# Performance work log

Hardware: AMD Instinct MI355X
Metric: run time of the kernel (lower is better)

Reference implementation:

```python
import jax, jax.numpy as jnp
import numpy as np

# --- fixed model configuration (from init_kwargs) ---
Nx, Nu, Ny, Np = 3, 1, 2, 5
Nz = Np * (Ny + Nu)          # 15
F, V, DELTA = 0.1, 1.0, 1.0  # ps (flow), volume, sampling time
CAMEAN, CBMEAN = 0.5, 0.4    # yscale means
CASTD, CBSTD = 0.3, 0.2      # yscale stds
CAFMEAN, CAFSTD = 1.0, 0.5   # uscale


def _fnn(x, W1, b1, W2, b2):
    # dense(tanh) -> dense(linear), as createDenseLayers/fnnTf
    return jnp.tanh(x @ W1 + b1) @ W2 + b2


def setup_inputs() -> dict:
    B, T = 4096, 1024
    key = jax.random.key(0)
    ks = jax.random.split(key, 16)
    g = lambda k, shp, fan: (jax.random.normal(k, shp, jnp.float32) / np.sqrt(fan))
    return {
        "u": jax.random.normal(ks[0], (B, T, Nu), jnp.float32),
        "xz0": jax.random.normal(ks[1], (B, Nx + Nz), jnp.float32),
        "r1_W1": g(ks[2], (1, 16), 1),  "r1_b1": jnp.zeros((16,), jnp.float32),
        "r1_W2": g(ks[3], (16, 1), 16), "r1_b2": jnp.zeros((1,), jnp.float32),
        "r2_W1": g(ks[4], (2, 16), 2),  "r2_b1": jnp.zeros((16,), jnp.float32),
        "r2_W2": g(ks[5], (16, 1), 16), "r2_b2": jnp.zeros((1,), jnp.float32),
        "eC_W1": g(ks[6], (Nz, 32), Nz), "eC_b1": jnp.zeros((32,), jnp.float32),
        "eC_W2": g(ks[7], (32, 1), 32),  "eC_b2": jnp.zeros((1,), jnp.float32),
    }


def _forward(u, xz0, r1_W1, r1_b1, r1_W2, r1_b2,
             r2_W1, r2_b1, r2_W2, r2_b2, eC_W1, eC_b1, eC_W2, eC_b2):

    def fxu(x, uu):
        Ca, Cb, Cc = x[:, 0:1], x[:, 1:2], x[:, 2:3]
        Caf = uu[:, 0:1]
        r1 = _fnn(Ca, r1_W1, r1_b1, r1_W2, r1_b2) * CASTD
        r2 = _fnn(jnp.concatenate((Cb, Cc), -1), r2_W1, r2_b1, r2_W2, r2_b2) * CBSTD
        Ca = Ca * CASTD + CAMEAN
        Cb = Cb * CBSTD + CBMEAN
        Cc = Cc * CBSTD + CBMEAN
        Caf = Caf * CAFSTD + CAFMEAN
        dCa = F * (Caf - Ca) / V - r1
        dCb = -F * Cb / V + r1 - 3.0 * r2
        dCc = -F * Cc / V + r2
        return jnp.concatenate([dCa / CASTD, dCb / CBSTD, dCc / CBSTD], -1)

    # initial state: replace Cc with NN estimate from past data z0
    y0 = xz0[:, :Ny]
    z0 = xz0[:, Nx:]
    Cc0 = _fnn(z0, eC_W1, eC_b1, eC_W2, eC_b2)
    xz = jnp.concatenate((y0, Cc0, z0), -1)  # [B, Nx+Nz]

    def step(xz, uu):
        x, z = xz[:, :Nx], xz[:, Nx:]
        ypseq, upseq = z[:, :Np * Ny], z[:, Np * Ny:]
        k1 = fxu(x, uu)
        k2 = fxu(x + DELTA * (k1 / 2.0), uu)
        k3 = fxu(x + DELTA * (k2 / 2.0), uu)
        k4 = fxu(x + DELTA * k3, uu)
        xplus = x + (DELTA / 6.0) * (k1 + 2.0 * k2 + 2.0 * k3 + k4)
        zplus = jnp.concatenate((ypseq[:, Ny:], x[:, :Ny], upseq[:, Nu:], uu), -1)
        CcNN = _fnn(z, eC_W1, eC_b1, eC_W2, eC_b2)
        y = jnp.concatenate((x, CcNN), -1)  # [B, Nx+1]
        return jnp.concatenate((xplus, zplus), -1), y

    u_t = jnp.swapaxes(u, 0, 1)  # [T, B, Nu]
    _, ys = jax.lax.scan(step, xz, u_t)
    yseq_full = jnp.swapaxes(ys, 0, 1)      # [B, T, Nx+1]
    yseq = yseq_full[..., :Ny]
    xseq = yseq_full[..., :Nx]
    return yseq_full, yseq, xseq


def reference(u, xz0, r1_W1, r1_b1, r1_W2, r1_b2,
              r2_W1, r2_b1, r2_W2, r2_b2, eC_W1, eC_b1, eC_W2, eC_b2):
    return _forward(u, xz0, r1_W1, r1_b1, r1_W2, r1_b2,
                    r2_W1, r2_b1, r2_W2, r2_b2, eC_W1, eC_b1, eC_W2, eC_b2)
```

## Files before the change

kernel.cpp:

```cpp
#include <hip/hip_runtime.h>
#include <stdint.h>
#include <math.h>

#define NB 4096
#define NT 1024


#if __has_builtin(__builtin_amdgcn_exp2f)
#define EXP2F __builtin_amdgcn_exp2f
#else
#define EXP2F exp2f
#endif
#if __has_builtin(__builtin_amdgcn_rcpf)
#define RCPF __builtin_amdgcn_rcpf
#else
#define RCPF(x) (1.0f / (x))
#endif

#define TS 2.885390081777927f

typedef float f32x2 __attribute__((ext_vector_type(2)));
__device__ __forceinline__ f32x2 sp2(float s) { return (f32x2){s, s}; }
#define FMA2(a, b, c) __builtin_elementwise_fma((a), (b), (c))

template <int CTRL>
__device__ __forceinline__ float dppmov(float x) {
  return __int_as_float(
      __builtin_amdgcn_update_dpp(0, __float_as_int(x), CTRL, 0xF, 0xF, true));
}

__global__ __launch_bounds__(64) void phase1_kernel(
    const float* __restrict__ u, const float* __restrict__ xz0,
    const float* __restrict__ r1W1, const float* __restrict__ r1b1,
    const float* __restrict__ r1W2, const float* __restrict__ r1b2,
    const float* __restrict__ r2W1, const float* __restrict__ r2b1,
    const float* __restrict__ r2W2, const float* __restrict__ r2b2,
    const float* __restrict__ eCW1, const float* __restrict__ eCb1,
    const float* __restrict__ eCW2, const float* __restrict__ eCb2,
    float* __restrict__ out) {
  const int tid = threadIdx.x;
  const int cl = tid & 7;
  const int q = tid & 3;
  const bool isQ1 = (tid & 4) != 0;
  const int chain = (blockIdx.x << 3) + (tid >> 3);

  f32x2 wAv0, wAv1, wBv0, wBv1, wCv0, wCv1, wPn2v0, wPn2v1;
  float wPsum;
  {
    float wa[4], wb[4], wc[4], wp[4];
#pragma unroll
    for (int m = 0; m < 4; ++m) {
      const int un = q + 4 * m;
      if (!isQ1) {
        wa[m] = r1W1[un] * TS;
        wb[m] = 0.0f;
        wc[m] = r1b1[un] * TS;
        wp[m] = r1W2[un];
      } else {
        wa[m] = r2W1[un] * TS;
        wb[m] = r2W1[16 + un] * TS;
        wc[m] = r2b1[un] * TS;
        wp[m] = r2W2[un];
      }
    }
    wAv0 = (f32x2){wa[0], wa[1]};
    wAv1 = (f32x2){wa[2], wa[3]};
    wBv0 = (f32x2){wb[0], wb[1]};
    wBv1 = (f32x2){wb[2], wb[3]};
    wCv0 = (f32x2){wc[0], wc[1]};
    wCv1 = (f32x2){wc[2], wc[3]};
    wPn2v0 = (f32x2){-2.0f * wp[0], -2.0f * wp[1]};
    wPn2v1 = (f32x2){-2.0f * wp[2], -2.0f * wp[3]};
    wPsum = wp[0] + wp[1] + wp[2] + wp[3];
  }
  const f32x2 wPh = {wPsum, 0.0f};
  const f32x2 zero2 = {0.0f, 0.0f};

  const f32x2 cwAh0 = 0.5f * wAv0, cwAh1 = 0.5f * wAv1;
  const f32x2 cwAf0 = wAv0, cwAf1 = wAv1;
  const f32x2 cwBh0 = 0.5f * wBv0, cwBh1 = 0.5f * wBv1;
  const f32x2 cwBf0 = wBv0, cwBf1 = wBv1;
  const f32x2 eOWNh0 =
      isQ1 ? (0.5f * wBv0 - 1.5f * wAv0) : (-0.5f * wAv0);
  const f32x2 eOWNh1 =
      isQ1 ? (0.5f * wBv1 - 1.5f * wAv1) : (-0.5f * wAv1);
  const f32x2 eOWNf0 = isQ1 ? (wBv0 - 3.0f * wAv0) : (-wAv0);
  const f32x2 eOWNf1 = isQ1 ? (wBv1 - 3.0f * wAv1) : (-wAv1);
  const f32x2 eOTHh0 = isQ1 ? (0.75f * wAv0) : zero2;
  const f32x2 eOTHh1 = isQ1 ? (0.75f * wAv1) : zero2;
  const f32x2 eOTHf0 = isQ1 ? (1.5f * wAv0) : zero2;
  const f32x2 eOTHf1 = isQ1 ? (1.5f * wAv1) : zero2;

  const float c1 = r1b2[0];
  const float c2 = r2b2[0];
  const float C0b = 1.0f / 6.0f - c1;
  const float C1 = -0.2f + 1.5f * c1 - 3.0f * c2;
  const float C2 = c2 - 0.2f;

  const float* xzr = xz0 + chain * 18;
  float x0 = xzr[0];
  float x1 = xzr[1];
  float x2;

  {
    float eh[4], ewn2[4];
    float ewsum = 0.0f;
#pragma unroll
    for (int m = 0; m < 4; ++m) {
      const int un = 4 * cl + m;
      eh[m] = eCb1[un];
      ewn2[m] = -2.0f * eCW2[un];
      ewsum += eCW2[un];
    }
#pragma unroll
    for (int i = 0; i < 15; ++i) {
      const float z = xzr[3 + i];
#pragma unroll
      for (int m = 0; m < 4; ++m)
        eh[m] = __builtin_fmaf(z, eCW1[i * 32 + 4 * cl + m], eh[m]);
    }
    float pl = ewsum;
#pragma unroll
    for (int m = 0; m < 4; ++m) {
      const float e = EXP2F(eh[m] * TS);
      const float r = RCPF(e + 1.0f);
      pl = __builtin_fmaf(ewn2[m], r, pl);
    }
    pl += dppmov<0xB1>(pl);
    pl += dppmov<0x4E>(pl);
    pl = pl + dppmov<0x141>(pl);
    x2 = pl + eCb2[0];
  }

  size_t idx0;
  int stride;
  if (cl < 3) {
    idx0 = (size_t)chain * NT * 4 + cl;
    stride = 4;
  } else if (cl < 5) {
    idx0 = (size_t)NB * NT * 4 + (size_t)chain * NT * 2 + (cl - 3);
    stride = 2;
  } else {
    idx0 = (size_t)NB * NT * 6 + (size_t)chain * NT * 3 + (cl - 5);
    stride = 3;
  }
  float* sp = out + idx0;
  const bool selx0 = (cl == 0) || (cl == 3) || (cl == 5);
  const bool selx1 = (cl == 1) || (cl == 4) || (cl == 6);

  auto nets = [&](f32x2 h0, f32x2 h1, float& Sown, float& Soth) {
    f32x2 e0, e1, r01, r23;
    e0.x = EXP2F(h0.x);
    e0.y = EXP2F(h0.y);
    e1.x = EXP2F(h1.x);
    e1.y = EXP2F(h1.y);
    e0 = e0 + sp2(1.0f);
    e1 = e1 + sp2(1.0f);
    r01.x = RCPF(e0.x);
    r01.y = RCPF(e0.y);
    r23.x = RCPF(e1.x);
    r23.y = RCPF(e1.y);
    f32x2 acc = FMA2(wPn2v0, r01, wPh);
    acc = FMA2(wPn2v1, r23, acc);
    float pl = acc.x + acc.y;
    pl += dppmov<0xB1>(pl);
    pl += dppmov<0x4E>(pl);
    Sown = pl;
    Soth = dppmov<0x141>(pl);
  };

  const float* urow = u + (size_t)chain * NT;
  float4 ucur = *(const float4*)urow;
  for (int t4 = 0; t4 < NT; t4 += 4) {
    const int tn = (t4 + 4 < NT) ? (t4 + 4) : (NT - 4);
    const float4 unext = *(const float4*)(urow + tn);
    const float us4[4] = {ucur.x, ucur.y, ucur.z, ucur.w};
#pragma unroll
    for (int e = 0; e < 4; ++e) {
      const float v = selx0 ? x0 : (selx1 ? x1 : x2);
      *sp = v;
      sp += stride;
      const float C0t = __builtin_fmaf(us4[e], 1.0f / 6.0f, C0b);
      const float U0 = __builtin_fmaf(-0.1f, x0, C0t);
      const float U1 = __builtin_fmaf(-0.1f, x1, C1);
      const float U2 = __builtin_fmaf(-0.1f, x2, C2);
      const float sU = isQ1 ? x1 : x0;
      const float sV = isQ1 ? x2 : x0;
      const f32x2 hx0 = FMA2(sp2(sU), wAv0, FMA2(sp2(sV), wBv0, wCv0));
      const f32x2 hx1 = FMA2(sp2(sU), wAv1, FMA2(sp2(sV), wBv1, wCv1));
      float So, St, S1, S2;
      nets(hx0, hx1, So, St);
      S1 = isQ1 ? St : So;
      S2 = isQ1 ? So : St;
      const float k10 = U0 - S1;
      const float k11 =
          __builtin_fmaf(1.5f, S1, __builtin_fmaf(-3.0f, S2, U1));
      const float k12 = U2 + S2;
      {
        const float Ua = isQ1 ? U1 : U0;
        const f32x2 p0 = FMA2(cwAh0, sp2(Ua), FMA2(cwBh0, sp2(U2), hx0));
        const f32x2 p1 = FMA2(cwAh1, sp2(Ua), FMA2(cwBh1, sp2(U2), hx1));
        const f32x2 h0 = FMA2(eOTHh0, sp2(St), FMA2(eOWNh0, sp2(So), p0));
        const f32x2 h1 = FMA2(eOTHh1, sp2(St), FMA2(eOWNh1, sp2(So), p1));
        nets(h0, h1, So, St);
      }
      const float U0_2 = __builtin_fmaf(-0.05f, k10, U0);
      const float U1_2 = __builtin_fmaf(-0.05f, k11, U1);
      const float U2_2 = __builtin_fmaf(-0.05f, k12, U2);
      S1 = isQ1 ? St : So;
      S2 = isQ1 ? So : St;
      const float k20 = U0_2 - S1;
      const float k21 =
          __builtin_fmaf(1.5f, S1, __builtin_fmaf(-3.0f, S2, U1_2));
      const float k22 = U2_2 + S2;
      {
        const float Ua = isQ1 ? U1_2 : U0_2;
        const f32x2 p0 = FMA2(cwAh0, sp2(Ua), FMA2(cwBh0, sp2(U2_2), hx0));
        const f32x2 p1 = FMA2(cwAh1, sp2(Ua), FMA2(cwBh1, sp2(U2_2), hx1));
        const f32x2 h0 = FMA2(eOTHh0, sp2(St), FMA2(eOWNh0, sp2(So), p0));
        const f32x2 h1 = FMA2(eOTHh1, sp2(St), FMA2(eOWNh1, sp2(So), p1));
        nets(h0, h1, So, St);
      }
      const float U0_3 = __builtin_fmaf(-0.05f, k20, U0);
      const float U1_3 = __builtin_fmaf(-0.05f, k21, U1);
      const float U2_3 = __builtin_fmaf(-0.05f, k22, U2);
      S1 = isQ1 ? St : So;
      S2 = isQ1 ? So : St;
      const float k30 = U0_3 - S1;
      const float k31 =
          __builtin_fmaf(1.5f, S1, __builtin_fmaf(-3.0f, S2, U1_3));
      const float k32 = U2_3 + S2;
      {
        const float Ua = isQ1 ? U1_3 : U0_3;
        const f32x2 p0 = FMA2(cwAf0, sp2(Ua), FMA2(cwBf0, sp2(U2_3), hx0));
        const f32x2 p1 = FMA2(cwAf1, sp2(Ua), FMA2(cwBf1, sp2(U2_3), hx1));
        const f32x2 h0 = FMA2(eOTHf0, sp2(St), FMA2(eOWNf0, sp2(So), p0));
        const f32x2 h1 = FMA2(eOTHf1, sp2(St), FMA2(eOWNf1, sp2(So), p1));
        nets(h0, h1, So, St);
      }
      const float U0_4 = __builtin_fmaf(-0.1f, k30, U0);
      const float U1_4 = __builtin_fmaf(-0.1f, k31, U1);
      const float U2_4 = __builtin_fmaf(-0.1f, k32, U2);
      S1 = isQ1 ? St : So;
      S2 = isQ1 ? So : St;
      const float k40 = U0_4 - S1;
      const float k41 =
          __builtin_fmaf(1.5f, S1, __builtin_fmaf(-3.0f, S2, U1_4));
      const float k42 = U2_4 + S2;
      float tA = k20 + k30;
      tA = __builtin_fmaf(2.0f, tA, k10) + k40;
      x0 = __builtin_fmaf(1.0f / 6.0f, tA, x0);
      float tB = k21 + k31;
      tB = __builtin_fmaf(2.0f, tB, k11) + k41;
      x1 = __builtin_fmaf(1.0f / 6.0f, tB, x1);
      float tC = k22 + k32;
      tC = __builtin_fmaf(2.0f, tC, k12) + k42;
      x2 = __builtin_fmaf(1.0f / 6.0f, tC, x2);
    }
    ucur = unext;
  }
}

__global__ __launch_bounds__(256) void phase2_kernel(
    const float* __restrict__ u, const float* __restrict__ xz0,
    const float* __restrict__ eCW1, const float* __restrict__ eCb1,
    const float* __restrict__ eCW2, const float* __restrict__ eCb2,
    float* __restrict__ out) {
  __shared__ float lw[32][16];
  __shared__ float lw2[32];
  const int tid = threadIdx.x;
  if (tid < 32) {
#pragma unroll
    for (int i = 0; i < 15; ++i) lw[tid][i] = eCW1[i * 32 + tid] * TS;
    lw[tid][15] = eCb1[tid] * TS;
    lw2[tid] = -2.0f * eCW2[tid];
  }
  __syncthreads();

  const int b = blockIdx.x;
  const int t0 = tid << 2;
  const float2* ysrow =
      (const float2*)(out + (size_t)NB * NT * 4) + (size_t)b * NT;
  const float* urow = u + (size_t)b * NT;
  const float* xzr = xz0 + b * 18;

  float yw[16], uw[8];
#pragma unroll
  for (int idx = 0; idx < 8; ++idx) {
    const int tp = t0 - 5 + idx;
    float a, c, uu;
    if (tp >= 0) {
      const float2 h = ysrow[tp];
      a = h.x;
      c = h.y;
      uu = urow[tp];
    } else {
      a = xzr[3 + 2 * (tp + 5)];
      c = xzr[4 + 2 * (tp + 5)];
      uu = xzr[13 + (tp + 5)];
    }
    yw[2 * idx] = a;
    yw[2 * idx + 1] = c;
    uw[idx] = uu;
  }

  float acc[4] = {0.f, 0.f, 0.f, 0.f};
  for (int j = 0; j < 32; ++j) {
    const float4 wa = ((const float4*)lw[j])[0];
    const float4 wb = ((const float4*)lw[j])[1];
    const float4 wc = ((const float4*)lw[j])[2];
    const float4 wd = ((const float4*)lw[j])[3];
    const float w2n = lw2[j];
#pragma unroll
    for (int e = 0; e < 4; ++e) {
      float h = wd.w;
      h = __builtin_fmaf(yw[2 * e + 0], wa.x, h);
      h = __builtin_fmaf(yw[2 * e + 1], wa.y, h);
      h = __builtin_fmaf(yw[2 * e + 2], wa.z, h);
      h = __builtin_fmaf(yw[2 * e + 3], wa.w, h);
      h = __builtin_fmaf(yw[2 * e + 4], wb.x, h);
      h = __builtin_fmaf(yw[2 * e + 5], wb.y, h);
      h = __builtin_fmaf(yw[2 * e + 6], wb.z, h);
      h = __builtin_fmaf(yw[2 * e + 7], wb.w, h);
      h = __builtin_fmaf(yw[2 * e + 8], wc.x, h);
      h = __builtin_fmaf(yw[2 * e + 9], wc.y, h);
      h = __builtin_fmaf(uw[e + 0], wc.z, h);
      h = __builtin_fmaf(uw[e + 1], wc.w, h);
      h = __builtin_fmaf(uw[e + 2], wd.x, h);
      h = __builtin_fmaf(uw[e + 3], wd.y, h);
      h = __builtin_fmaf(uw[e + 4], wd.z, h);
      const float r = RCPF(EXP2F(h) + 1.0f);
      acc[e] = __builtin_fmaf(w2n, r, acc[e]);
    }
  }
  float sw = 0.0f;
#pragma unroll
  for (int j = 0; j < 32; ++j) sw += eCW2[j];
  const float C = eCb2[0] + sw;
  float* yfrow = out + (size_t)b * NT * 4;
#pragma unroll
  for (int e = 0; e < 4; ++e) {
    yfrow[(t0 + e) * 4 + 3] = acc[e] + C;
  }
}

extern "C" void kernel_launch(void* const* d_in, const int* in_sizes, int n_in,
                              void* d_out, int out_size, void* d_ws,
                              size_t ws_size, hipStream_t stream) {
  const float* u = (const float*)d_in[0];
  const float* xz0 = (const float*)d_in[1];
  const float* r1W1 = (const float*)d_in[2];
  const float* r1b1 = (const float*)d_in[3];
  const float* r1W2 = (const float*)d_in[4];
  const float* r1b2 = (const float*)d_in[5];
  const float* r2W1 = (const float*)d_in[6];
  const float* r2b1 = (const float*)d_in[7];
  const float* r2W2 = (const float*)d_in[8];
  const float* r2b2 = (const float*)d_in[9];
  const float* eCW1 = (const float*)d_in[10];
  const float* eCb1 = (const float*)d_in[11];
  const float* eCW2 = (const float*)d_in[12];
  const float* eCb2 = (const float*)d_in[13];
  float* out = (float*)d_out;

  hipLaunchKernelGGL(phase1_kernel, dim3(NB / 8), dim3(64), 0, stream, u, xz0,
                     r1W1, r1b1, r1W2, r1b2, r2W1, r2b1, r2W2, r2b2, eCW1,
                     eCb1, eCW2, eCb2, out);
  hipLaunchKernelGGL(phase2_kernel, dim3(NB), dim3(256), 0, stream, u, xz0,
                     eCW1, eCb1, eCW2, eCb2, out);
}
```

Measured before the change: 591.7 us.

## Shorten RK4 critical path by folding network outputs into next-stage preactivations

Restructures the RK4 recurrence so each stage's hidden preactivation is built from the parts that do not depend on the previous net output, then updated with a short FMA chain once that output arrives. The k4 contribution to the next state is split algebraically, so the next step's first-stage preactivation and U terms are formed from partial sums plus a 1/6-scaled correction. This is meant to cut the serial dependency latency between successive network evaluations in the sequential scan. In exchange it carries more live registers across iterations and slightly changes floating-point rounding order.

```diff
diff --git a/kernel.cpp b/kernel.cpp
--- a/kernel.cpp
+++ b/kernel.cpp
@@ -77,19 +77,15 @@
   const f32x2 zero2 = {0.0f, 0.0f};
 
   const f32x2 cwAh0 = 0.5f * wAv0, cwAh1 = 0.5f * wAv1;
-  const f32x2 cwAf0 = wAv0, cwAf1 = wAv1;
   const f32x2 cwBh0 = 0.5f * wBv0, cwBh1 = 0.5f * wBv1;
-  const f32x2 cwBf0 = wBv0, cwBf1 = wBv1;
-  const f32x2 eOWNh0 =
-      isQ1 ? (0.5f * wBv0 - 1.5f * wAv0) : (-0.5f * wAv0);
-  const f32x2 eOWNh1 =
-      isQ1 ? (0.5f * wBv1 - 1.5f * wAv1) : (-0.5f * wAv1);
   const f32x2 eOWNf0 = isQ1 ? (wBv0 - 3.0f * wAv0) : (-wAv0);
   const f32x2 eOWNf1 = isQ1 ? (wBv1 - 3.0f * wAv1) : (-wAv1);
-  const f32x2 eOTHh0 = isQ1 ? (0.75f * wAv0) : zero2;
-  const f32x2 eOTHh1 = isQ1 ? (0.75f * wAv1) : zero2;
   const f32x2 eOTHf0 = isQ1 ? (1.5f * wAv0) : zero2;
   const f32x2 eOTHf1 = isQ1 ? (1.5f * wAv1) : zero2;
+  const f32x2 eOWNh0 = 0.5f * eOWNf0, eOWNh1 = 0.5f * eOWNf1;
+  const f32x2 eOTHh0 = 0.5f * eOTHf0, eOTHh1 = 0.5f * eOTHf1;
+  const f32x2 eOWN60 = (1.0f / 6.0f) * eOWNf0, eOWN61 = (1.0f / 6.0f) * eOWNf1;
+  const f32x2 eOTH60 = (1.0f / 6.0f) * eOTHf0, eOTH61 = (1.0f / 6.0f) * eOTHf1;
 
   const float c1 = r1b2[0];
   const float c2 = r2b2[0];
@@ -171,6 +167,22 @@
 
   const float* urow = u + (size_t)chain * NT;
   float4 ucur = *(const float4*)urow;
+
+  float U0 = __builtin_fmaf(-0.1f, x0,
+                            __builtin_fmaf(ucur.x, 1.0f / 6.0f, C0b));
+  float U1 = __builtin_fmaf(-0.1f, x1, C1);
+  float U2 = __builtin_fmaf(-0.1f, x2, C2);
+  f32x2 h1v0, h1v1, pre2v0, pre2v1;
+  {
+    const float sU = isQ1 ? x1 : x0;
+    const float sV = isQ1 ? x2 : x0;
+    h1v0 = FMA2(wAv0, sp2(sU), FMA2(wBv0, sp2(sV), wCv0));
+    h1v1 = FMA2(wAv1, sp2(sU), FMA2(wBv1, sp2(sV), wCv1));
+    const float Ua = isQ1 ? U1 : U0;
+    pre2v0 = FMA2(cwAh0, sp2(Ua), FMA2(cwBh0, sp2(U2), h1v0));
+    pre2v1 = FMA2(cwAh1, sp2(Ua), FMA2(cwBh1, sp2(U2), h1v1));
+  }
+
   for (int t4 = 0; t4 < NT; t4 += 4) {
     const int tn = (t4 + 4 < NT) ? (t4 + 4) : (NT - 4);
     const float4 unext = *(const float4*)(urow + tn);
@@ -180,82 +192,81 @@
       const float v = selx0 ? x0 : (selx1 ? x1 : x2);
       *sp = v;
       sp += stride;
-      const float C0t = __builtin_fmaf(us4[e], 1.0f / 6.0f, C0b);
-      const float U0 = __builtin_fmaf(-0.1f, x0, C0t);
-      const float U1 = __builtin_fmaf(-0.1f, x1, C1);
-      const float U2 = __builtin_fmaf(-0.1f, x2, C2);
-      const float sU = isQ1 ? x1 : x0;
-      const float sV = isQ1 ? x2 : x0;
-      const f32x2 hx0 = FMA2(sp2(sU), wAv0, FMA2(sp2(sV), wBv0, wCv0));
-      const f32x2 hx1 = FMA2(sp2(sU), wAv1, FMA2(sp2(sV), wBv1, wCv1));
+      const float unx = (e < 3) ? us4[e + 1] : unext.x;
       float So, St, S1, S2;
-      nets(hx0, hx1, So, St);
+      nets(h1v0, h1v1, So, St);
+      const f32x2 h2v0 = FMA2(eOTHh0, sp2(St), FMA2(eOWNh0, sp2(So), pre2v0));
+      const f32x2 h2v1 = FMA2(eOTHh1, sp2(St), FMA2(eOWNh1, sp2(So), pre2v1));
       S1 = isQ1 ? St : So;
       S2 = isQ1 ? So : St;
       const float k10 = U0 - S1;
       const float k11 =
           __builtin_fmaf(1.5f, S1, __builtin_fmaf(-3.0f, S2, U1));
       const float k12 = U2 + S2;
-      {
-        const float Ua = isQ1 ? U1 : U0;
-        const f32x2 p0 = FMA2(cwAh0, sp2(Ua), FMA2(cwBh0, sp2(U2), hx0));
-        const f32x2 p1 = FMA2(cwAh1, sp2(Ua), FMA2(cwBh1, sp2(U2), hx1));
-        const f32x2 h0 = FMA2(eOTHh0, sp2(St), FMA2(eOWNh0, sp2(So), p0));
-        const f32x2 h1 = FMA2(eOTHh1, sp2(St), FMA2(eOWNh1, sp2(So), p1));
-        nets(h0, h1, So, St);
-      }
       const float U0_2 = __builtin_fmaf(-0.05f, k10, U0);
       const float U1_2 = __builtin_fmaf(-0.05f, k11, U1);
       const float U2_2 = __builtin_fmaf(-0.05f, k12, U2);
+      const float Ua2 = isQ1 ? U1_2 : U0_2;
+      const f32x2 pre3v0 = FMA2(cwAh0, sp2(Ua2), FMA2(cwBh0, sp2(U2_2), h1v0));
+      const f32x2 pre3v1 = FMA2(cwAh1, sp2(Ua2), FMA2(cwBh1, sp2(U2_2), h1v1));
+      nets(h2v0, h2v1, So, St);
+      const f32x2 h3v0 = FMA2(eOTHh0, sp2(St), FMA2(eOWNh0, sp2(So), pre3v0));
+      const f32x2 h3v1 = FMA2(eOTHh1, sp2(St), FMA2(eOWNh1, sp2(So), pre3v1));
       S1 = isQ1 ? St : So;
       S2 = isQ1 ? So : St;
       const float k20 = U0_2 - S1;
       const float k21 =
           __builtin_fmaf(1.5f, S1, __builtin_fmaf(-3.0f, S2, U1_2));
       const float k22 = U2_2 + S2;
-      {
-        const float Ua = isQ1 ? U1_2 : U0_2;
-        const f32x2 p0 = FMA2(cwAh0, sp2(Ua), FMA2(cwBh0, sp2(U2_2), hx0));
-        const f32x2 p1 = FMA2(cwAh1, sp2(Ua), FMA2(cwBh1, sp2(U2_2), hx1));
-        const f32x2 h0 = FMA2(eOTHh0, sp2(St), FMA2(eOWNh0, sp2(So), p0));
-        const f32x2 h1 = FMA2(eOTHh1, sp2(St), FMA2(eOWNh1, sp2(So), p1));
-        nets(h0, h1, So, St);
-      }
       const float U0_3 = __builtin_fmaf(-0.05f, k20, U0);
       const float U1_3 = __builtin_fmaf(-0.05f, k21, U1);
       const float U2_3 = __builtin_fmaf(-0.05f, k22, U2);
+      const float Ua3 = isQ1 ? U1_3 : U0_3;
+      const f32x2 pre4v0 = FMA2(wAv0, sp2(Ua3), FMA2(wBv0, sp2(U2_3), h1v0));
+      const f32x2 pre4v1 = FMA2(wAv1, sp2(Ua3), FMA2(wBv1, sp2(U2_3), h1v1));
+      nets(h3v0, h3v1, So, St);
+      const f32x2 h4v0 = FMA2(eOTHf0, sp2(St), FMA2(eOWNf0, sp2(So), pre4v0));
+      const f32x2 h4v1 = FMA2(eOTHf1, sp2(St), FMA2(eOWNf1, sp2(So), pre4v1));
       S1 = isQ1 ? St : So;
       S2 = isQ1 ? So : St;
       const float k30 = U0_3 - S1;
       const float k31 =
           __builtin_fmaf(1.5f, S1, __builtin_fmaf(-3.0f, S2, U1_3));
       const float k32 = U2_3 + S2;
-      {
-        const float Ua = isQ1 ? U1_3 : U0_3;
-        const f32x2 p0 = FMA2(cwAf0, sp2(Ua), FMA2(cwBf0, sp2(U2_3), hx0));
-        const f32x2 p1 = FMA2(cwAf1, sp2(Ua), FMA2(cwBf1, sp2(U2_3), hx1));
-        const f32x2 h0 = FMA2(eOTHf0, sp2(St), FMA2(eOWNf0, sp2(So), p0));
-        const f32x2 h1 = FMA2(eOTHf1, sp2(St), FMA2(eOWNf1, sp2(So), p1));
-        nets(h0, h1, So, St);
-      }
       const float U0_4 = __builtin_fmaf(-0.1f, k30, U0);
       const float U1_4 = __builtin_fmaf(-0.1f, k31, U1);
       const float U2_4 = __builtin_fmaf(-0.1f, k32, U2);
+      float q0 = k20 + k30;
+      const float Q0 = __builtin_fmaf(2.0f, q0, k10) + U0_4;
+      const float P0 = __builtin_fmaf(1.0f / 6.0f, Q0, x0);
+      float q1 = k21 + k31;
+      const float Q1 = __builtin_fmaf(2.0f, q1, k11) + U1_4;
+      const float P1 = __builtin_fmaf(1.0f / 6.0f, Q1, x1);
+      float q2 = k22 + k32;
+      const float Q2 = __builtin_fmaf(2.0f, q2, k12) + U2_4;
+      const float P2 = __builtin_fmaf(1.0f / 6.0f, Q2, x2);
+      const float C0tn = __builtin_fmaf(unx, 1.0f / 6.0f, C0b);
+      const float pU0 = __builtin_fmaf(-0.1f, P0, C0tn);
+      const float pU1 = __builtin_fmaf(-0.1f, P1, C1);
+      const float pU2 = __builtin_fmaf(-0.1f, P2, C2);
+      const float Pa = isQ1 ? P1 : P0;
+      const float Pv = isQ1 ? P2 : P0;
+      const f32x2 preHv0 = FMA2(wAv0, sp2(Pa), FMA2(wBv0, sp2(Pv), wCv0));
+      const f32x2 preHv1 = FMA2(wAv1, sp2(Pa), FMA2(wBv1, sp2(Pv), wCv1));
+      nets(h4v0, h4v1, So, St);
+      h1v0 = FMA2(eOTH60, sp2(St), FMA2(eOWN60, sp2(So), preHv0));
+      h1v1 = FMA2(eOTH61, sp2(St), FMA2(eOWN61, sp2(So), preHv1));
       S1 = isQ1 ? St : So;
       S2 = isQ1 ? So : St;
-      const float k40 = U0_4 - S1;
-      const float k41 =
-          __builtin_fmaf(1.5f, S1, __builtin_fmaf(-3.0f, S2, U1_4));
-      const float k42 = U2_4 + S2;
-      float tA = k20 + k30;
-      tA = __builtin_fmaf(2.0f, tA, k10) + k40;
-      x0 = __builtin_fmaf(1.0f / 6.0f, tA, x0);
-      float tB = k21 + k31;
-      tB = __builtin_fmaf(2.0f, tB, k11) + k41;
-      x1 = __builtin_fmaf(1.0f / 6.0f, tB, x1);
-      float tC = k22 + k32;
-      tC = __builtin_fmaf(2.0f, tC, k12) + k42;
-      x2 = __builtin_fmaf(1.0f / 6.0f, tC, x2);
+      x0 = __builtin_fmaf(-1.0f / 6.0f, S1, P0);
+      x1 = __builtin_fmaf(0.25f, S1, __builtin_fmaf(-0.5f, S2, P1));
+      x2 = __builtin_fmaf(1.0f / 6.0f, S2, P2);
+      U0 = __builtin_fmaf(1.0f / 60.0f, S1, pU0);
+      U1 = __builtin_fmaf(-0.025f, S1, __builtin_fmaf(0.05f, S2, pU1));
+      U2 = __builtin_fmaf(-1.0f / 60.0f, S2, pU2);
+      const float Ua = isQ1 ? U1 : U0;
+      pre2v0 = FMA2(cwAh0, sp2(Ua), FMA2(cwBh0, sp2(U2), h1v0));
+      pre2v1 = FMA2(cwAh1, sp2(Ua), FMA2(cwBh1, sp2(U2), h1v1));
     }
     ucur = unext;
   }
```

Result: no change. 581.8 us (-1.7%).
